# Performance work log

Measured on AMD Instinct MI355X. Metric: run time of the kernel, lower is better.

Reference implementation:

```python
import jax, jax.numpy as jnp
import numpy as np

N_FEATS = 9       # OGB atom feature columns
VOCAB = 119       # per-feature embedding vocab (max OGB atom vocab)
HIDDEN = 128
NUM_HEADS = 8
HEAD_DIM = HIDDEN // NUM_HEADS


def setup_inputs() -> dict:
    key = jax.random.key(0)
    ks = jax.random.split(key, 12)
    N, K = 50000, 16
    X = jax.random.randint(ks[0], (N, N_FEATS), 0, VOCAB)
    nbr_idx = jax.random.randint(ks[1], (N, K), 0, N)
    nbr_mask = jax.random.randint(ks[2], (N, K), 0, 2).astype(bool)
    atom_emb = jax.random.normal(ks[3], (N_FEATS, VOCAB, HIDDEN), jnp.float32) * 0.02
    s = 1.0 / np.sqrt(HIDDEN)
    Wq = jax.random.normal(ks[4], (HIDDEN, HIDDEN), jnp.float32) * s
    bq = jnp.zeros((HIDDEN,), jnp.float32)
    Wk = jax.random.normal(ks[5], (HIDDEN, HIDDEN), jnp.float32) * s
    bk = jnp.zeros((HIDDEN,), jnp.float32)
    Wv = jax.random.normal(ks[6], (HIDDEN, HIDDEN), jnp.float32) * s
    bv = jnp.zeros((HIDDEN,), jnp.float32)
    return {"X": X, "nbr_idx": nbr_idx, "nbr_mask": nbr_mask,
            "atom_emb": atom_emb, "Wq": Wq, "bq": bq,
            "Wk": Wk, "bk": bk, "Wv": Wv, "bv": bv}


def reference(X, nbr_idx, nbr_mask, atom_emb, Wq, bq, Wk, bk, Wv, bv):
    N = X.shape[0]
    # AtomEncoder: sum per-feature embedding lookups -> [N, HIDDEN]
    h = jnp.sum(atom_emb[jnp.arange(N_FEATS)[None, :], X], axis=1)
    scaling = HEAD_DIM ** -0.5
    q = (h @ Wq + bq).reshape(N, NUM_HEADS, HEAD_DIM) * scaling
    k = (h @ Wk + bk).reshape(N, NUM_HEADS, HEAD_DIM)
    v = (h @ Wv + bv).reshape(N, NUM_HEADS, HEAD_DIM)
    # ELL-format sparse attention: gather padded neighbor k/v -> [N, K, H, D]
    k_n = k[nbr_idx]
    v_n = v[nbr_idx]
    scores = jnp.einsum('nhd,nkhd->nkh', q, k_n)          # [N, K, H]
    scores = jnp.where(nbr_mask[..., None], scores, -1e9)
    attn = jax.nn.softmax(scores, axis=1)                 # softmax over neighbors
    out = jnp.einsum('nkh,nkhd->nhd', attn, v_n)          # [N, H, D]
    return out.reshape(N, HIDDEN)
```

## Files before the change

### kernel.cpp

```cpp
#include <hip/hip_runtime.h>
#include <hip/hip_bf16.h>

#define NFEAT 9
#define VOCAB 119
#define HIDDEN 128
#define NHEAD 8
#define HDIM 16
#define KNBR 16

typedef __attribute__((ext_vector_type(8))) short short8;
typedef __attribute__((ext_vector_type(4))) float f32x4;

__device__ __forceinline__ void load_lds16(const void* g, void* l) {
    __builtin_amdgcn_global_load_lds((const __attribute__((address_space(1))) void*)g,
                                     (__attribute__((address_space(3))) void*)l, 16, 0, 0);
}

__global__ void fill_kernel(float* out, int n, float val) {
    int i = blockIdx.x * blockDim.x + threadIdx.x;
    if (i < n) out[i] = val;
}

__global__ __launch_bounds__(256) void wt_kernel(
    const float* __restrict__ Wq, const float* __restrict__ Wk,
    const float* __restrict__ Wv, short* __restrict__ Wt)
{
    int mat = blockIdx.x >> 2, tile = blockIdx.x & 3;
    const float* W = (mat == 0) ? Wq : (mat == 1) ? Wk : Wv;
    __shared__ float ls[32 * HIDDEN];
    int tid = threadIdx.x;
    int cc0 = tile * 32;
    #pragma unroll
    for (int j = 0; j < 16; ++j) {
        int idx = j * 256 + tid;
        ls[idx] = W[(size_t)cc0 * HIDDEN + idx];
    }
    __syncthreads();
    int c = tid & 127, hf = tid >> 7;
    unsigned int ob[8];
    #pragma unroll
    for (int j = 0; j < 8; ++j) {
        int ccl = hf * 16 + 2 * j;
        __hip_bfloat16 b0 = __float2bfloat16(ls[ccl * HIDDEN + c]);
        __hip_bfloat16 b1 = __float2bfloat16(ls[(ccl + 1) * HIDDEN + c]);
        ob[j] = (unsigned int)*reinterpret_cast<unsigned short*>(&b0)
              | ((unsigned int)*reinterpret_cast<unsigned short*>(&b1) << 16);
    }
    unsigned int* dst = reinterpret_cast<unsigned int*>(
        Wt + (size_t)mat * HIDDEN * HIDDEN + (size_t)c * HIDDEN + cc0 + hf * 16);
    #pragma unroll
    for (int j = 0; j < 8; ++j) dst[j] = ob[j];
}

#define MT 32
#define HBS 136

__global__ __launch_bounds__(256, 4) void qkv_kernel(
    const int* __restrict__ X, const float* __restrict__ emb,
    const short* __restrict__ Wt,
    const float* __restrict__ bq, const float* __restrict__ bk,
    const float* __restrict__ bv,
    float* __restrict__ qf, __hip_bfloat16* __restrict__ kv, int N)
{
    __shared__ __align__(16) short hb[MT * HBS];
    __shared__ int xs[MT * NFEAT];

    const int tid = threadIdx.x;
    const int n0 = blockIdx.x * MT;

    for (int i = tid; i < MT * NFEAT; i += 256) {
        int n = n0 + i / NFEAT;
        int v = (n < N) ? X[(size_t)n * NFEAT + (i % NFEAT)] : 0;
        xs[i] = min(max(v, 0), VOCAB - 1);
    }
    __syncthreads();

    {
        const int cg = tid & 31;
        const int slot = tid >> 5;
        #pragma unroll
        for (int i = 0; i < 4; ++i) {
            int nl = slot * 4 + i;
            float4 acc = {0.f, 0.f, 0.f, 0.f};
            #pragma unroll
            for (int f = 0; f < NFEAT; ++f) {
                const float4 e = *reinterpret_cast<const float4*>(
                    &emb[((size_t)f * VOCAB + xs[nl * NFEAT + f]) * HIDDEN + cg * 4]);
                acc.x += e.x; acc.y += e.y; acc.z += e.z; acc.w += e.w;
            }
            __hip_bfloat162 p0 = __float22bfloat162_rn(make_float2(acc.x, acc.y));
            __hip_bfloat162 p1 = __float22bfloat162_rn(make_float2(acc.z, acc.w));
            uint2 u;
            u.x = *reinterpret_cast<unsigned int*>(&p0);
            u.y = *reinterpret_cast<unsigned int*>(&p1);
            *reinterpret_cast<uint2*>(&hb[nl * HBS + cg * 4]) = u;
        }
    }
    __syncthreads();

    const int wave = tid >> 6, lane = tid & 63;
    const int l15 = lane & 15, quad = lane >> 4;
    const int mtile = wave & 1, nthalf = wave >> 1;
    const int mloc = mtile * 16 + l15;

    short8 a[4];
    #pragma unroll
    for (int k0 = 0; k0 < 4; ++k0)
        a[k0] = *reinterpret_cast<const short8*>(&hb[mloc * HBS + k0 * 32 + quad * 8]);

    #pragma unroll
    for (int nt = 0; nt < 4; ++nt) {
        const int ntg = nthalf * 4 + nt;
        const int n = ntg * 16 + l15;
        short8 b[3][4];
        #pragma unroll
        for (int mat = 0; mat < 3; ++mat)
            #pragma unroll
            for (int k0 = 0; k0 < 4; ++k0)
                b[mat][k0] = *reinterpret_cast<const short8*>(
                    &Wt[(size_t)mat * HIDDEN * HIDDEN + n * HIDDEN + k0 * 32 + quad * 8]);
        f32x4 acc[3] = {{0.f,0.f,0.f,0.f},{0.f,0.f,0.f,0.f},{0.f,0.f,0.f,0.f}};
        #pragma unroll
        for (int mat = 0; mat < 3; ++mat)
            #pragma unroll
            for (int k0 = 0; k0 < 4; ++k0)
                acc[mat] = __builtin_amdgcn_mfma_f32_16x16x32_bf16(
                    a[k0], b[mat][k0], acc[mat], 0, 0, 0);
        float bb[3] = {bq[n], bk[n], bv[n]};
        #pragma unroll
        for (int mat = 0; mat < 3; ++mat) {
            #pragma unroll
            for (int r = 0; r < 4; ++r) {
                int node = n0 + mtile * 16 + quad * 4 + r;
                if (node < N) {
                    float val = acc[mat][r] + bb[mat];
                    if (mat == 0)      qf[(size_t)node * HIDDEN + n] = val * 0.25f;
                    else if (mat == 1) kv[(size_t)node * 256 + n] = __float2bfloat16(val);
                    else               kv[(size_t)node * 256 + 128 + n] = __float2bfloat16(val);
                }
            }
        }
    }
}

#define NPB2 2

__global__ __launch_bounds__(256) void attn_kernel(
    const int* __restrict__ nbr_idx, const int* __restrict__ nbr_mask,
    const float* __restrict__ qf, const __hip_bfloat16* __restrict__ kv,
    float* __restrict__ out, int N)
{
    __shared__ __align__(16) __hip_bfloat16 kvl[NPB2][KNBR][256];
    __shared__ float ql[NPB2][HIDDEN];
    __shared__ float sl[NPB2][KNBR][NHEAD + 1];
    __shared__ float el[NPB2][KNBR][NHEAD + 1];
    __shared__ int idxl[NPB2][KNBR];
    __shared__ int mskl[NPB2][KNBR];

    const int tid = threadIdx.x;
    const int local = tid >> 7;
    const int t = tid & 127;
    int n = blockIdx.x * NPB2 + local;
    if (n >= N) n = N - 1;

    ql[local][t] = qf[(size_t)n * HIDDEN + t];
    if (t < KNBR) {
        int iv = nbr_idx[(size_t)n * KNBR + t];
        idxl[local][t] = min(max(iv, 0), N - 1);
        mskl[local][t] = nbr_mask[(size_t)n * KNBR + t];
    }
    __syncthreads();

    {
        const int w2 = t >> 6;
        const int l = t & 63;
        #pragma unroll
        for (int j = 0; j < 4; ++j) {
            int r = 4 * j + 2 * w2 + (l >> 5);
            const short* src = (const short*)kv
                + (size_t)idxl[local][r] * 256 + (size_t)(l & 31) * 8;
            load_lds16(src, &kvl[local][4 * j + 2 * w2][0]);
        }
    }
    __syncthreads();

    const int kk = t >> 3, hh = t & 7;
    float s = 0.f;
    {
        const __hip_bfloat162* kp =
            reinterpret_cast<const __hip_bfloat162*>(&kvl[local][kk][hh * HDIM]);
        const float* qp = &ql[local][hh * HDIM];
        #pragma unroll
        for (int d2 = 0; d2 < HDIM / 2; ++d2) {
            float2 kf = __bfloat1622float2(kp[d2]);
            s += qp[2 * d2] * kf.x + qp[2 * d2 + 1] * kf.y;
        }
    }
    if (!mskl[local][kk]) s = -1e9f;
    sl[local][kk][hh] = s;
    __syncthreads();

    float mx = -3.0e38f;
    #pragma unroll
    for (int j = 0; j < KNBR; ++j) mx = fmaxf(mx, sl[local][j][hh]);
    float e = __expf(s - mx);
    el[local][kk][hh] = e;
    __syncthreads();
    float denom = 0.f;
    #pragma unroll
    for (int j = 0; j < KNBR; ++j) denom += el[local][j][hh];
    sl[local][kk][hh] = e / denom;
    __syncthreads();

    const int h2 = t >> 4, dd = t & 15;
    float o = 0.f;
    #pragma unroll
    for (int j = 0; j < KNBR; ++j) {
        float a = sl[local][j][h2];
        float vv = __bfloat162float(kvl[local][j][HIDDEN + h2 * HDIM + dd]);
        o += a * vv;
    }
    out[(size_t)n * HIDDEN + t] = o;
}

extern "C" void kernel_launch(void* const* d_in, const int* in_sizes, int n_in,
                              void* d_out, int out_size, void* d_ws, size_t ws_size,
                              hipStream_t stream)
{
    float* out = (float*)d_out;

    bool ok = (n_in == 10);
    int N = ok ? in_sizes[0] / NFEAT : 0;
    ok = ok && N > 0 && in_sizes[0] == N * NFEAT
            && in_sizes[1] == N * KNBR
            && in_sizes[2] == N * KNBR
            && in_sizes[3] == NFEAT * VOCAB * HIDDEN
            && in_sizes[4] == HIDDEN * HIDDEN && in_sizes[5] == HIDDEN
            && in_sizes[6] == HIDDEN * HIDDEN && in_sizes[7] == HIDDEN
            && in_sizes[8] == HIDDEN * HIDDEN && in_sizes[9] == HIDDEN
            && out_size == N * HIDDEN;
    if (!ok) {
        fill_kernel<<<(out_size + 255) / 256, 256, 0, stream>>>(out, out_size, 0.0f);
        return;
    }
    size_t need = (size_t)N * 1024 + 3 * HIDDEN * HIDDEN * sizeof(short);
    if (ws_size < need) {
        fill_kernel<<<(out_size + 255) / 256, 256, 0, stream>>>(out, out_size, 1.0f);
        return;
    }

    const int* X        = (const int*)d_in[0];
    const int* nbr_idx  = (const int*)d_in[1];
    const int* nbr_mask = (const int*)d_in[2];
    const float* emb = (const float*)d_in[3];
    const float* Wq  = (const float*)d_in[4];
    const float* bq  = (const float*)d_in[5];
    const float* Wk  = (const float*)d_in[6];
    const float* bk  = (const float*)d_in[7];
    const float* Wv  = (const float*)d_in[8];
    const float* bv  = (const float*)d_in[9];

    float* qf = (float*)d_ws;
    __hip_bfloat16* kv =
        (__hip_bfloat16*)((char*)d_ws + (size_t)N * HIDDEN * sizeof(float));
    short* Wt = (short*)((char*)d_ws + (size_t)N * 1024);

    wt_kernel<<<12, 256, 0, stream>>>(Wq, Wk, Wv, Wt);
    qkv_kernel<<<(N + MT - 1) / MT, 256, 0, stream>>>(
        X, emb, Wt, bq, bk, bv, qf, kv, N);
    attn_kernel<<<(N + NPB2 - 1) / NPB2, 256, 0, stream>>>(
        nbr_idx, nbr_mask, qf, kv, out, N);
}
```

Baseline: 196.1 us.

## Skip masked neighbor K gathers and fuse softmax with V accumulation in registers

The attention kernel no longer issues K-row gathers for masked neighbors; it still loads their V rows. The gathered K/V rows are stored as padded row pairs in LDS, and each thread keeps its head's q slice in registers instead of staging it through LDS. The softmax max, exp, sum and V-weighted sum now run in one register pass per thread, which removes two barriers and the separate exp buffer. The aim is to cut gather bandwidth and synchronization, at the cost of more registers per thread and a masked-lane branch in the load loop.

Result: faster. 186.6 us (-4.9%).

```diff
diff --git a/kernel.cpp b/kernel.cpp
--- a/kernel.cpp
+++ b/kernel.cpp
@@ -144,16 +144,15 @@
 }
 
 #define NPB2 2
+#define PAIRW 520
 
 __global__ __launch_bounds__(256) void attn_kernel(
     const int* __restrict__ nbr_idx, const int* __restrict__ nbr_mask,
     const float* __restrict__ qf, const __hip_bfloat16* __restrict__ kv,
     float* __restrict__ out, int N)
 {
-    __shared__ __align__(16) __hip_bfloat16 kvl[NPB2][KNBR][256];
-    __shared__ float ql[NPB2][HIDDEN];
+    __shared__ __align__(16) __hip_bfloat16 kvp[NPB2][8][PAIRW];
     __shared__ float sl[NPB2][KNBR][NHEAD + 1];
-    __shared__ float el[NPB2][KNBR][NHEAD + 1];
     __shared__ int idxl[NPB2][KNBR];
     __shared__ int mskl[NPB2][KNBR];
 
@@ -163,7 +162,6 @@
     int n = blockIdx.x * NPB2 + local;
     if (n >= N) n = N - 1;
 
-    ql[local][t] = qf[(size_t)n * HIDDEN + t];
     if (t < KNBR) {
         int iv = nbr_idx[(size_t)n * KNBR + t];
         idxl[local][t] = min(max(iv, 0), N - 1);
@@ -171,56 +169,78 @@
     }
     __syncthreads();
 
+    const int hh = t >> 4;
+    const int kk = t & 15;
+
+    float qr[HDIM];
+    {
+        const float4* qp = reinterpret_cast<const float4*>(
+            qf + (size_t)n * HIDDEN + hh * HDIM);
+        #pragma unroll
+        for (int c4 = 0; c4 < 4; ++c4) {
+            float4 qv = qp[c4];
+            qr[4 * c4 + 0] = qv.x; qr[4 * c4 + 1] = qv.y;
+            qr[4 * c4 + 2] = qv.z; qr[4 * c4 + 3] = qv.w;
+        }
+    }
+
     {
         const int w2 = t >> 6;
         const int l = t & 63;
         #pragma unroll
         for (int j = 0; j < 4; ++j) {
-            int r = 4 * j + 2 * w2 + (l >> 5);
-            const short* src = (const short*)kv
-                + (size_t)idxl[local][r] * 256 + (size_t)(l & 31) * 8;
-            load_lds16(src, &kvl[local][4 * j + 2 * w2][0]);
-        }
-    }
-    __syncthreads();
-
-    const int kk = t >> 3, hh = t & 7;
-    float s = 0.f;
-    {
-        const __hip_bfloat162* kp =
-            reinterpret_cast<const __hip_bfloat162*>(&kvl[local][kk][hh * HDIM]);
-        const float* qp = &ql[local][hh * HDIM];
-        #pragma unroll
-        for (int d2 = 0; d2 < HDIM / 2; ++d2) {
-            float2 kf = __bfloat1622float2(kp[d2]);
-            s += qp[2 * d2] * kf.x + qp[2 * d2 + 1] * kf.y;
-        }
-    }
-    if (!mskl[local][kk]) s = -1e9f;
-    sl[local][kk][hh] = s;
-    __syncthreads();
-
-    float mx = -3.0e38f;
-    #pragma unroll
-    for (int j = 0; j < KNBR; ++j) mx = fmaxf(mx, sl[local][j][hh]);
-    float e = __expf(s - mx);
-    el[local][kk][hh] = e;
-    __syncthreads();
-    float denom = 0.f;
-    #pragma unroll
-    for (int j = 0; j < KNBR; ++j) denom += el[local][j][hh];
-    sl[local][kk][hh] = e / denom;
-    __syncthreads();
-
-    const int h2 = t >> 4, dd = t & 15;
-    float o = 0.f;
-    #pragma unroll
-    for (int j = 0; j < KNBR; ++j) {
-        float a = sl[local][j][h2];
-        float vv = __bfloat162float(kvl[local][j][HIDDEN + h2 * HDIM + dd]);
-        o += a * vv;
-    }
-    out[(size_t)n * HIDDEN + t] = o;
+            int pair = 2 * j + w2;
+            int r = pair * 2 + (l >> 5);
+            bool khalf = (l & 31) < 16;
+            if (!khalf || mskl[local][r]) {
+                const short* src = (const short*)kv
+                    + (size_t)idxl[local][r] * 256 + (size_t)(l & 31) * 8;
+                load_lds16(src, &kvp[local][pair][0]);
+            }
+        }
+    }
+    __syncthreads();
+
+    {
+        const short8* kb = reinterpret_cast<const short8*>(
+            &kvp[local][kk >> 1][(kk & 1) * 256 + hh * HDIM]);
+        short8 k0 = kb[0], k1 = kb[1];
+        const __hip_bfloat162* kp0 = reinterpret_cast<const __hip_bfloat162*>(&k0);
+        const __hip_bfloat162* kp1 = reinterpret_cast<const __hip_bfloat162*>(&k1);
+        float s = 0.f;
+        #pragma unroll
+        for (int d2 = 0; d2 < 4; ++d2) {
+            float2 f0 = __bfloat1622float2(kp0[d2]);
+            float2 f1 = __bfloat1622float2(kp1[d2]);
+            s += qr[2 * d2] * f0.x + qr[2 * d2 + 1] * f0.y;
+            s += qr[8 + 2 * d2] * f1.x + qr[8 + 2 * d2 + 1] * f1.y;
+        }
+        if (!mskl[local][kk]) s = -1e9f;
+        sl[local][kk][hh] = s;
+    }
+    __syncthreads();
+
+    {
+        const int dd = kk;
+        float sj[KNBR];
+        #pragma unroll
+        for (int j = 0; j < KNBR; ++j) sj[j] = sl[local][j][hh];
+        float mx = sj[0];
+        #pragma unroll
+        for (int j = 1; j < KNBR; ++j) mx = fmaxf(mx, sj[j]);
+        float e[KNBR], denom = 0.f;
+        #pragma unroll
+        for (int j = 0; j < KNBR; ++j) { e[j] = __expf(sj[j] - mx); denom += e[j]; }
+        float inv = 1.f / denom;
+        float o = 0.f;
+        #pragma unroll
+        for (int j = 0; j < KNBR; ++j) {
+            float vv = __bfloat162float(
+                kvp[local][j >> 1][(j & 1) * 256 + HIDDEN + hh * HDIM + dd]);
+            o += e[j] * vv;
+        }
+        out[(size_t)n * HIDDEN + t] = o * inv;
+    }
 }
 
 extern "C" void kernel_launch(void* const* d_in, const int* in_sizes, int n_in,
```
